# Performance work log

Measured on AMD Instinct MI355X. Metric: run time of the kernel, lower is better.

The kernel has to match this reference:

```python
import jax, jax.numpy as jnp
from jax import lax
import numpy as np

B, DIM, L_IN = 8, 512, 4096
SCALE = 2
KSIZE = 17
DN = ('NCH', 'OIH', 'NCH')  # conv1d dimension numbers


def _aa_kernel(kernel_size: int, scale: int) -> np.ndarray:
    # replicates scipy.signal.kaiser_atten / kaiser_beta / windows.kaiser
    atten = 2.285 * (kernel_size - 1) * np.pi * (1.0 / scale) + 7.95
    if atten > 50:
        beta = 0.1102 * (atten - 8.7)
    elif atten > 21:
        beta = 0.5842 * (atten - 21) ** 0.4 + 0.07886 * (atten - 21)
    else:
        beta = 0.0
    win = np.kaiser(kernel_size, beta)
    xk = np.arange(kernel_size) - kernel_size // 2
    k = np.sinc(xk / scale) * win  # normalized sinc, same as torch.sinc
    return (k / k.sum()).astype(np.float32)


def setup_inputs() -> dict:
    key = jax.random.key(0)
    k1, k2, k3, k4, k5 = jax.random.split(key, 5)
    kconv = 2 * SCALE - 1
    return {
        'x': jax.random.normal(k1, (B, DIM, L_IN), dtype=jnp.float32),
        'conv_w': jax.random.normal(k2, (DIM, DIM, kconv), dtype=jnp.float32) * (1.0 / np.sqrt(DIM * kconv)),
        'conv_b': jax.random.normal(k3, (DIM,), dtype=jnp.float32) * 0.01,
        'aa_kernel': jnp.asarray(_aa_kernel(KSIZE, SCALE)),
        'proj_w': jax.random.normal(k4, (DIM, DIM), dtype=jnp.float32) * (1.0 / np.sqrt(DIM)),
        'proj_b': jax.random.normal(k5, (DIM,), dtype=jnp.float32) * 0.01,
    }


def reference(x, conv_w, conv_b, aa_kernel, proj_w, proj_b):
    s = SCALE
    # zero-insertion upsample + Conv1d(dim,dim,2s-1,pad=s-1) fused via lhs_dilation.
    # Torch zero-inserts to length l*s (trailing s-1 zeros), so right pad is 2s-2.
    y = lax.conv_general_dilated(
        x, conv_w, window_strides=(1,), padding=[(s - 1, 2 * s - 2)],
        lhs_dilation=(s,), dimension_numbers=DN,
    ) + conv_b[None, :, None]  # [B, D, l*s]
    # depthwise anti-alias filter (same Kaiser-sinc kernel per channel)
    dw = jnp.broadcast_to(aa_kernel, (DIM, 1, KSIZE))
    y = lax.conv_general_dilated(
        y, dw, window_strides=(1,), padding=[(KSIZE // 2, KSIZE // 2)],
        feature_group_count=DIM, dimension_numbers=DN,
    )
    # pointwise 1x1 projection
    return jnp.einsum('bdl,ed->bel', y, proj_w) + proj_b[None, :, None]
```

## Files before the change

### kernel.cpp

```cpp
#include <hip/hip_runtime.h>
#include <hip/hip_bf16.h>

#define BB_   8
#define DIM_  512
#define LIN_  4096
#define LOUT_ 8192

typedef __attribute__((ext_vector_type(8))) __bf16 bf16x8;
typedef __attribute__((ext_vector_type(4))) float  f32x4;

__device__ __forceinline__ void async_copy16(const void* g, void* l) {
  __builtin_amdgcn_global_load_lds(
      (__attribute__((address_space(1))) void*)g,
      (__attribute__((address_space(3))) void*)l, 16, 0, 0);
}

__global__ __launch_bounds__(256) void k_transpose(const float* __restrict__ x,
                                                   __hip_bfloat16* __restrict__ Xt) {
  __shared__ float t[64][65];
  const int b  = blockIdx.x;
  const int d0 = blockIdx.y * 64;
  const int l0 = blockIdx.z * 64;
  const int tid = threadIdx.x;
  const int jj = tid & 63;
  const int i0 = tid >> 6;
#pragma unroll
  for (int r = 0; r < 16; ++r) {
    const int i = i0 + r * 4;
    t[i][jj] = x[(size_t)(b * DIM_ + d0 + i) * LIN_ + l0 + jj];
  }
  __syncthreads();
#pragma unroll
  for (int r = 0; r < 16; ++r) {
    const int i = i0 + r * 4;
    Xt[(size_t)(b * LIN_ + l0 + i) * DIM_ + d0 + jj] = __float2bfloat16(t[jj][i]);
  }
}

__global__ __launch_bounds__(256) void k_prep(const float* __restrict__ proj_w,
                                              const float* __restrict__ conv_w,
                                              __hip_bfloat16* __restrict__ Mst) {
  const int kk = blockIdx.x;
  const int et = blockIdx.y * 32;
  const int it = blockIdx.z * 32;
  __shared__ float Pt[32][33];
  __shared__ float Wt[32][33];
  const int tid = threadIdx.x;
  const int tx = tid & 15, ty = tid >> 4;
  float acc[2][2] = {};
  for (int d0 = 0; d0 < DIM_; d0 += 32) {
    {
      const int i = tid >> 3;
      const int j = (tid & 7) * 4;
      const float4 v = *(const float4*)&proj_w[(size_t)(et + i) * DIM_ + d0 + j];
      Pt[i][j] = v.x; Pt[i][j + 1] = v.y; Pt[i][j + 2] = v.z; Pt[i][j + 3] = v.w;
    }
#pragma unroll
    for (int r = 0; r < 4; ++r) {
      const int idx = tid + r * 256;
      const int i = idx >> 5, j = idx & 31;
      Wt[i][j] = conv_w[(size_t)(d0 + i) * (DIM_ * 3) + (it + j) * 3 + kk];
    }
    __syncthreads();
#pragma unroll
    for (int dl = 0; dl < 32; ++dl) {
      float pv[2], wv[2];
      pv[0] = Pt[ty * 2][dl];     pv[1] = Pt[ty * 2 + 1][dl];
      wv[0] = Wt[dl][tx * 2];     wv[1] = Wt[dl][tx * 2 + 1];
#pragma unroll
      for (int a = 0; a < 2; ++a)
#pragma unroll
        for (int bq = 0; bq < 2; ++bq) acc[a][bq] += pv[a] * wv[bq];
    }
    __syncthreads();
  }
#pragma unroll
  for (int a = 0; a < 2; ++a)
#pragma unroll
    for (int bq = 0; bq < 2; ++bq)
      Mst[(size_t)(kk * DIM_ + et + ty * 2 + a) * DIM_ + it + tx * 2 + bq] =
          __float2bfloat16(acc[a][bq]);
}

__global__ __launch_bounds__(64) void k_pcb(const float* __restrict__ proj_w,
                                            const float* __restrict__ conv_b,
                                            float* __restrict__ Pcb) {
  const int e = blockIdx.x;
  const int j = threadIdx.x;
  float s = 0.f;
#pragma unroll
  for (int d = j; d < DIM_; d += 64) s += proj_w[(size_t)e * DIM_ + d] * conv_b[d];
#pragma unroll
  for (int off = 32; off > 0; off >>= 1) s += __shfl_down(s, off, 64);
  if (j == 0) Pcb[e] = s;
}

__global__ __launch_bounds__(256) void k_gemm(const __hip_bfloat16* __restrict__ A,
                                              const __hip_bfloat16* __restrict__ Bt,
                                              const float* __restrict__ Pcb,
                                              __hip_bfloat16* __restrict__ U) {
  __shared__ __align__(16) __hip_bfloat16 As[128 * 64];
  __shared__ __align__(16) __hip_bfloat16 Bs[128 * 64];
  const int tid = threadIdx.x;
  const int r0 = blockIdx.x * 128;
  const int c0 = blockIdx.y * 128;
  const int lane = tid & 63;
  const int wave = tid >> 6;
  const int wm = wave >> 1, wn = wave & 1;

  const int srow = tid >> 3;
  const int cg   = (tid & 7) ^ (srow & 7);
  const __hip_bfloat16* aptr = A  + (size_t)(r0 + srow) * 512 + cg * 8;
  const __hip_bfloat16* bptr = Bt + (size_t)(c0 + srow) * 512 + cg * 8;
  __hip_bfloat16* ldsA = As + tid * 8;
  __hip_bfloat16* ldsB = Bs + tid * 8;

  f32x4 acc[4][4] = {};

  const int kq   = lane >> 4;
  const int mrow = wm * 64 + (lane & 15);
  const int ncol = wn * 64 + (lane & 15);

  for (int kt = 0; kt < 512; kt += 64) {
#pragma unroll
    for (int it = 0; it < 4; ++it) {
      async_copy16(aptr + (size_t)(it * 32) * 512 + kt, ldsA + it * 2048);
      async_copy16(bptr + (size_t)(it * 32) * 512 + kt, ldsB + it * 2048);
    }
    __syncthreads();
#pragma unroll
    for (int k0 = 0; k0 < 64; k0 += 32) {
      const int c = (k0 >> 3) + kq;
      bf16x8 af[4], bfr[4];
#pragma unroll
      for (int i = 0; i < 4; ++i) {
        const int rg = mrow + i * 16;
        af[i] = *(const bf16x8*)(As + rg * 64 + ((c ^ (rg & 7)) * 8));
      }
#pragma unroll
      for (int i = 0; i < 4; ++i) {
        const int rg = ncol + i * 16;
        bfr[i] = *(const bf16x8*)(Bs + rg * 64 + ((c ^ (rg & 7)) * 8));
      }
#pragma unroll
      for (int mt = 0; mt < 4; ++mt)
#pragma unroll
        for (int nt = 0; nt < 4; ++nt)
          acc[mt][nt] = __builtin_amdgcn_mfma_f32_16x16x32_bf16(af[mt], bfr[nt],
                                                                acc[mt][nt], 0, 0, 0);
    }
    __syncthreads();
  }

  const int kk = r0 >> 9;
  const int bb = c0 >> 12;
  const int e0 = (r0 & 511) + wm * 64;
  const int l0 = (c0 & 4095) + wn * 64;
#pragma unroll
  for (int mt = 0; mt < 4; ++mt) {
#pragma unroll
    for (int nt = 0; nt < 4; ++nt) {
      const int ltile = l0 + nt * 16 + (lane & 15);
      const int ebase = e0 + mt * 16 + (lane >> 4) * 4;
#pragma unroll
      for (int r = 0; r < 4; ++r) {
        float v = acc[mt][nt][r];
        const int e = ebase + r;
        if (kk < 2) v += Pcb[e];
        U[(size_t)((kk * 8 + bb) * 512 + e) * 4096 + ltile] = __float2bfloat16(v);
      }
    }
  }
}

__global__ __launch_bounds__(256) void k_aa(const __hip_bfloat16* __restrict__ U,
                                            const float* __restrict__ aa,
                                            const float* __restrict__ proj_b,
                                            float* __restrict__ out) {
  const int b  = blockIdx.x >> 9;
  const int e  = blockIdx.x & 511;
  const int l0 = blockIdx.y << 10;
  __shared__ __align__(16) float ue[1040];
  __shared__ __align__(16) float uo[1040];
  __shared__ float sa[17];
  const int tid = threadIdx.x;
  if (tid < 17) sa[tid] = aa[tid];
  const __hip_bfloat16* U0 = U + (size_t)((0 * 8 + b) * 512 + e) * 4096;
  const __hip_bfloat16* U1 = U + (size_t)((1 * 8 + b) * 512 + e) * 4096;
  const __hip_bfloat16* U2 = U + (size_t)((2 * 8 + b) * 512 + e) * 4096;
  for (int s = tid; s < 1040; s += 256) {
    const int l = l0 - 8 + s;
    float ve = 0.f, vo = 0.f;
    if (l >= 0 && l < 4096) {
      ve = __bfloat162float(U1[l]);
      vo = __bfloat162float(U0[l]);
      if (l + 1 < 4096) vo += __bfloat162float(U2[l + 1]);
    }
    ue[s] = ve;
    uo[s] = vo;
  }
  __syncthreads();
  const float pb = proj_b[e];
  const int li0 = tid * 4;
  const int w0  = li0 + 4;
  float Ew[12], Ow[12];
#pragma unroll
  for (int c = 0; c < 3; ++c) {
    const float4 ve = *(const float4*)&ue[w0 + 4 * c];
    const float4 vo = *(const float4*)&uo[w0 + 4 * c];
    Ew[4 * c] = ve.x; Ew[4 * c + 1] = ve.y; Ew[4 * c + 2] = ve.z; Ew[4 * c + 3] = ve.w;
    Ow[4 * c] = vo.x; Ow[4 * c + 1] = vo.y; Ow[4 * c + 2] = vo.z; Ow[4 * c + 3] = vo.w;
  }
  float res[8];
#pragma unroll
  for (int t = 0; t < 4; ++t) {
    float se = 0.f, so = 0.f;
#pragma unroll
    for (int q = 0; q <= 8; ++q) {
      se += sa[2 * q] * Ew[t + q];
      so += sa[2 * q] * Ow[t + q];
    }
#pragma unroll
    for (int q = 0; q < 8; ++q) {
      se += sa[2 * q + 1] * Ow[t + q];
      so += sa[2 * q + 1] * Ew[t + q + 1];
    }
    res[2 * t]     = se + pb;
    res[2 * t + 1] = so + pb;
  }
  float* orow = out + (size_t)(b * 512 + e) * 8192 + 2 * (l0 + li0);
  *(float4*)(orow)     = *(float4*)&res[0];
  *(float4*)(orow + 4) = *(float4*)&res[4];
}

extern "C" void kernel_launch(void* const* d_in, const int* in_sizes, int n_in,
                              void* d_out, int out_size, void* d_ws, size_t ws_size,
                              hipStream_t stream) {
  const float* x      = (const float*)d_in[0];
  const float* conv_w = (const float*)d_in[1];
  const float* conv_b = (const float*)d_in[2];
  const float* aa     = (const float*)d_in[3];
  const float* proj_w = (const float*)d_in[4];
  const float* proj_b = (const float*)d_in[5];
  float* out = (float*)d_out;

  char* ws = (char*)d_ws;
  __hip_bfloat16* Xt  = (__hip_bfloat16*)ws;
  __hip_bfloat16* Mst = (__hip_bfloat16*)(ws + 33554432);
  float*          Pcb = (float*)(ws + 35127296);
  __hip_bfloat16* U   = (__hip_bfloat16*)(ws + 35129344);

  k_transpose<<<dim3(8, 8, 64), 256, 0, stream>>>(x, Xt);
  k_prep<<<dim3(3, 16, 16), 256, 0, stream>>>(proj_w, conv_w, Mst);
  k_pcb<<<dim3(512, 1, 1), 64, 0, stream>>>(proj_w, conv_b, Pcb);
  k_gemm<<<dim3(12, 256), 256, 0, stream>>>(Mst, Xt, Pcb, U);
  k_aa<<<dim3(4096, 4), 256, 0, stream>>>(U, aa, proj_b, out);
}
```

Before: 384.5 us.

## Merge prep kernels, double-buffer GEMM LDS via registers, drop LDS staging in AA

Three preprocessing kernels (transpose, weight premultiply, bias projection) are merged into one launch that dispatches on block index, saving two launches. The GEMM swaps direct global-to-LDS async copies for register-staged loads into double-buffered LDS, so the next K tile is fetched while the current one is computed, at the cost of more LDS and a launch bound of two blocks. The anti-alias kernel now reads the bf16 intermediate straight into registers with vector loads and a fast-path bounds check instead of staging through shared memory. The block-index dispatch in the merged kernel must stay exact, and the extra LDS may limit occupancy.

New measurement: 380.7 us. No clear change (-1.0%).

```diff
diff --git a/kernel.cpp b/kernel.cpp
--- a/kernel.cpp
+++ b/kernel.cpp
@@ -9,98 +9,101 @@
 typedef __attribute__((ext_vector_type(8))) __bf16 bf16x8;
 typedef __attribute__((ext_vector_type(4))) float  f32x4;
 
-__device__ __forceinline__ void async_copy16(const void* g, void* l) {
-  __builtin_amdgcn_global_load_lds(
-      (__attribute__((address_space(1))) void*)g,
-      (__attribute__((address_space(3))) void*)l, 16, 0, 0);
-}
-
-__global__ __launch_bounds__(256) void k_transpose(const float* __restrict__ x,
-                                                   __hip_bfloat16* __restrict__ Xt) {
-  __shared__ float t[64][65];
-  const int b  = blockIdx.x;
-  const int d0 = blockIdx.y * 64;
-  const int l0 = blockIdx.z * 64;
+__device__ __forceinline__ float bf2f(unsigned short u) {
+  union { unsigned int i; float f; } x;
+  x.i = ((unsigned int)u) << 16;
+  return x.f;
+}
+
+__global__ __launch_bounds__(256) void k_pre(const float* __restrict__ x,
+                                             const float* __restrict__ proj_w,
+                                             const float* __restrict__ conv_w,
+                                             const float* __restrict__ conv_b,
+                                             __hip_bfloat16* __restrict__ Xt,
+                                             __hip_bfloat16* __restrict__ Mst,
+                                             float* __restrict__ Pcb) {
+  __shared__ float smem[64 * 65];
+  const int bx  = blockIdx.x;
   const int tid = threadIdx.x;
-  const int jj = tid & 63;
-  const int i0 = tid >> 6;
-#pragma unroll
-  for (int r = 0; r < 16; ++r) {
-    const int i = i0 + r * 4;
-    t[i][jj] = x[(size_t)(b * DIM_ + d0 + i) * LIN_ + l0 + jj];
-  }
-  __syncthreads();
-#pragma unroll
-  for (int r = 0; r < 16; ++r) {
-    const int i = i0 + r * 4;
-    Xt[(size_t)(b * LIN_ + l0 + i) * DIM_ + d0 + jj] = __float2bfloat16(t[jj][i]);
-  }
-}
-
-__global__ __launch_bounds__(256) void k_prep(const float* __restrict__ proj_w,
-                                              const float* __restrict__ conv_w,
-                                              __hip_bfloat16* __restrict__ Mst) {
-  const int kk = blockIdx.x;
-  const int et = blockIdx.y * 32;
-  const int it = blockIdx.z * 32;
-  __shared__ float Pt[32][33];
-  __shared__ float Wt[32][33];
-  const int tid = threadIdx.x;
-  const int tx = tid & 15, ty = tid >> 4;
-  float acc[2][2] = {};
-  for (int d0 = 0; d0 < DIM_; d0 += 32) {
-    {
-      const int i = tid >> 3;
-      const int j = (tid & 7) * 4;
-      const float4 v = *(const float4*)&proj_w[(size_t)(et + i) * DIM_ + d0 + j];
-      Pt[i][j] = v.x; Pt[i][j + 1] = v.y; Pt[i][j + 2] = v.z; Pt[i][j + 3] = v.w;
-    }
-#pragma unroll
-    for (int r = 0; r < 4; ++r) {
-      const int idx = tid + r * 256;
-      const int i = idx >> 5, j = idx & 31;
-      Wt[i][j] = conv_w[(size_t)(d0 + i) * (DIM_ * 3) + (it + j) * 3 + kk];
+  if (bx < 4096) {
+    const int b  = bx & 7;
+    const int d0 = ((bx >> 3) & 7) * 64;
+    const int l0 = (bx >> 6) * 64;
+    const int jj = tid & 63;
+    const int i0 = tid >> 6;
+#pragma unroll
+    for (int r = 0; r < 16; ++r) {
+      const int i = i0 + r * 4;
+      smem[i * 65 + jj] = x[(size_t)(b * DIM_ + d0 + i) * LIN_ + l0 + jj];
     }
     __syncthreads();
 #pragma unroll
-    for (int dl = 0; dl < 32; ++dl) {
-      float pv[2], wv[2];
-      pv[0] = Pt[ty * 2][dl];     pv[1] = Pt[ty * 2 + 1][dl];
-      wv[0] = Wt[dl][tx * 2];     wv[1] = Wt[dl][tx * 2 + 1];
-#pragma unroll
-      for (int a = 0; a < 2; ++a)
-#pragma unroll
-        for (int bq = 0; bq < 2; ++bq) acc[a][bq] += pv[a] * wv[bq];
-    }
-    __syncthreads();
-  }
-#pragma unroll
-  for (int a = 0; a < 2; ++a)
-#pragma unroll
-    for (int bq = 0; bq < 2; ++bq)
-      Mst[(size_t)(kk * DIM_ + et + ty * 2 + a) * DIM_ + it + tx * 2 + bq] =
-          __float2bfloat16(acc[a][bq]);
-}
-
-__global__ __launch_bounds__(64) void k_pcb(const float* __restrict__ proj_w,
-                                            const float* __restrict__ conv_b,
-                                            float* __restrict__ Pcb) {
-  const int e = blockIdx.x;
-  const int j = threadIdx.x;
-  float s = 0.f;
-#pragma unroll
-  for (int d = j; d < DIM_; d += 64) s += proj_w[(size_t)e * DIM_ + d] * conv_b[d];
-#pragma unroll
-  for (int off = 32; off > 0; off >>= 1) s += __shfl_down(s, off, 64);
-  if (j == 0) Pcb[e] = s;
-}
-
-__global__ __launch_bounds__(256) void k_gemm(const __hip_bfloat16* __restrict__ A,
-                                              const __hip_bfloat16* __restrict__ Bt,
-                                              const float* __restrict__ Pcb,
-                                              __hip_bfloat16* __restrict__ U) {
-  __shared__ __align__(16) __hip_bfloat16 As[128 * 64];
-  __shared__ __align__(16) __hip_bfloat16 Bs[128 * 64];
+    for (int r = 0; r < 16; ++r) {
+      const int i = i0 + r * 4;
+      Xt[(size_t)(b * LIN_ + l0 + i) * DIM_ + d0 + jj] =
+          __float2bfloat16(smem[jj * 65 + i]);
+    }
+  } else if (bx < 4864) {
+    const int idx = bx - 4096;
+    const int kk = idx >> 8;
+    const int et = ((idx >> 4) & 15) * 32;
+    const int it = (idx & 15) * 32;
+    float* Pt = smem;
+    float* Wt = smem + 32 * 33;
+    const int tx = tid & 15, ty = tid >> 4;
+    float acc[2][2] = {};
+    for (int d0 = 0; d0 < DIM_; d0 += 32) {
+      {
+        const int i = tid >> 3;
+        const int j = (tid & 7) * 4;
+        const float4 v = *(const float4*)&proj_w[(size_t)(et + i) * DIM_ + d0 + j];
+        Pt[i * 33 + j] = v.x; Pt[i * 33 + j + 1] = v.y;
+        Pt[i * 33 + j + 2] = v.z; Pt[i * 33 + j + 3] = v.w;
+      }
+#pragma unroll
+      for (int r = 0; r < 4; ++r) {
+        const int id2 = tid + r * 256;
+        const int i = id2 >> 5, j = id2 & 31;
+        Wt[i * 33 + j] = conv_w[(size_t)(d0 + i) * (DIM_ * 3) + (it + j) * 3 + kk];
+      }
+      __syncthreads();
+#pragma unroll
+      for (int dl = 0; dl < 32; ++dl) {
+        float pv[2], wv[2];
+        pv[0] = Pt[(ty * 2) * 33 + dl];     pv[1] = Pt[(ty * 2 + 1) * 33 + dl];
+        wv[0] = Wt[dl * 33 + tx * 2];       wv[1] = Wt[dl * 33 + tx * 2 + 1];
+#pragma unroll
+        for (int a = 0; a < 2; ++a)
+#pragma unroll
+          for (int bq = 0; bq < 2; ++bq) acc[a][bq] += pv[a] * wv[bq];
+      }
+      __syncthreads();
+    }
+#pragma unroll
+    for (int a = 0; a < 2; ++a)
+#pragma unroll
+      for (int bq = 0; bq < 2; ++bq)
+        Mst[(size_t)(kk * DIM_ + et + ty * 2 + a) * DIM_ + it + tx * 2 + bq] =
+            __float2bfloat16(acc[a][bq]);
+  } else {
+    const int idx = bx - 4864;
+    const int e = idx * 4 + (tid >> 6);
+    const int j = tid & 63;
+    float s = 0.f;
+#pragma unroll
+    for (int d = j; d < DIM_; d += 64) s += proj_w[(size_t)e * DIM_ + d] * conv_b[d];
+#pragma unroll
+    for (int off = 32; off > 0; off >>= 1) s += __shfl_down(s, off, 64);
+    if (j == 0) Pcb[e] = s;
+  }
+}
+
+__global__ __launch_bounds__(256, 2) void k_gemm(const __hip_bfloat16* __restrict__ A,
+                                                 const __hip_bfloat16* __restrict__ Bt,
+                                                 const float* __restrict__ Pcb,
+                                                 __hip_bfloat16* __restrict__ U) {
+  __shared__ __align__(16) __hip_bfloat16 As[2][128 * 64];
+  __shared__ __align__(16) __hip_bfloat16 Bs[2][128 * 64];
   const int tid = threadIdx.x;
   const int r0 = blockIdx.x * 128;
   const int c0 = blockIdx.y * 128;
@@ -108,26 +111,45 @@
   const int wave = tid >> 6;
   const int wm = wave >> 1, wn = wave & 1;
 
-  const int srow = tid >> 3;
-  const int cg   = (tid & 7) ^ (srow & 7);
-  const __hip_bfloat16* aptr = A  + (size_t)(r0 + srow) * 512 + cg * 8;
-  const __hip_bfloat16* bptr = Bt + (size_t)(c0 + srow) * 512 + cg * 8;
-  __hip_bfloat16* ldsA = As + tid * 8;
-  __hip_bfloat16* ldsB = Bs + tid * 8;
+  const int rA = tid >> 3;
+  const int ch = tid & 7;
+  const __hip_bfloat16* aG = A  + (size_t)(r0 + rA) * 512 + ch * 8;
+  const __hip_bfloat16* bG = Bt + (size_t)(c0 + rA) * 512 + ch * 8;
+  int wo[4];
+#pragma unroll
+  for (int i = 0; i < 4; ++i) {
+    const int rg = rA + 32 * i;
+    wo[i] = rg * 64 + ((ch ^ (rg & 7)) * 8);
+  }
+
+  bf16x8 gA[4], gB[4];
+#pragma unroll
+  for (int i = 0; i < 4; ++i) {
+    gA[i] = *(const bf16x8*)(aG + (size_t)(32 * i) * 512);
+    gB[i] = *(const bf16x8*)(bG + (size_t)(32 * i) * 512);
+  }
+#pragma unroll
+  for (int i = 0; i < 4; ++i) {
+    *(bf16x8*)(&As[0][wo[i]]) = gA[i];
+    *(bf16x8*)(&Bs[0][wo[i]]) = gB[i];
+  }
+  __syncthreads();
 
   f32x4 acc[4][4] = {};
-
   const int kq   = lane >> 4;
   const int mrow = wm * 64 + (lane & 15);
   const int ncol = wn * 64 + (lane & 15);
 
-  for (int kt = 0; kt < 512; kt += 64) {
-#pragma unroll
-    for (int it = 0; it < 4; ++it) {
-      async_copy16(aptr + (size_t)(it * 32) * 512 + kt, ldsA + it * 2048);
-      async_copy16(bptr + (size_t)(it * 32) * 512 + kt, ldsB + it * 2048);
-    }
-    __syncthreads();
+  for (int kt = 0; kt < 8; ++kt) {
+    if (kt < 7) {
+#pragma unroll
+      for (int i = 0; i < 4; ++i) {
+        gA[i] = *(const bf16x8*)(aG + (size_t)(32 * i) * 512 + (kt + 1) * 64);
+        gB[i] = *(const bf16x8*)(bG + (size_t)(32 * i) * 512 + (kt + 1) * 64);
+      }
+    }
+    const __hip_bfloat16* Ab = As[kt & 1];
+    const __hip_bfloat16* Bb = Bs[kt & 1];
 #pragma unroll
     for (int k0 = 0; k0 < 64; k0 += 32) {
       const int c = (k0 >> 3) + kq;
@@ -135,12 +157,12 @@
 #pragma unroll
       for (int i = 0; i < 4; ++i) {
         const int rg = mrow + i * 16;
-        af[i] = *(const bf16x8*)(As + rg * 64 + ((c ^ (rg & 7)) * 8));
+        af[i] = *(const bf16x8*)(Ab + rg * 64 + ((c ^ (rg & 7)) * 8));
       }
 #pragma unroll
       for (int i = 0; i < 4; ++i) {
         const int rg = ncol + i * 16;
-        bfr[i] = *(const bf16x8*)(Bs + rg * 64 + ((c ^ (rg & 7)) * 8));
+        bfr[i] = *(const bf16x8*)(Bb + rg * 64 + ((c ^ (rg & 7)) * 8));
       }
 #pragma unroll
       for (int mt = 0; mt < 4; ++mt)
@@ -148,6 +170,15 @@
         for (int nt = 0; nt < 4; ++nt)
           acc[mt][nt] = __builtin_amdgcn_mfma_f32_16x16x32_bf16(af[mt], bfr[nt],
                                                                 acc[mt][nt], 0, 0, 0);
+    }
+    if (kt < 7) {
+      __hip_bfloat16* wA = &As[(kt + 1) & 1][0];
+      __hip_bfloat16* wB = &Bs[(kt + 1) & 1][0];
+#pragma unroll
+      for (int i = 0; i < 4; ++i) {
+        *(bf16x8*)(&wA[wo[i]]) = gA[i];
+        *(bf16x8*)(&wB[wo[i]]) = gB[i];
+      }
     }
     __syncthreads();
   }
@@ -180,37 +211,51 @@
   const int b  = blockIdx.x >> 9;
   const int e  = blockIdx.x & 511;
   const int l0 = blockIdx.y << 10;
-  __shared__ __align__(16) float ue[1040];
-  __shared__ __align__(16) float uo[1040];
-  __shared__ float sa[17];
   const int tid = threadIdx.x;
-  if (tid < 17) sa[tid] = aa[tid];
-  const __hip_bfloat16* U0 = U + (size_t)((0 * 8 + b) * 512 + e) * 4096;
-  const __hip_bfloat16* U1 = U + (size_t)((1 * 8 + b) * 512 + e) * 4096;
-  const __hip_bfloat16* U2 = U + (size_t)((2 * 8 + b) * 512 + e) * 4096;
-  for (int s = tid; s < 1040; s += 256) {
-    const int l = l0 - 8 + s;
-    float ve = 0.f, vo = 0.f;
-    if (l >= 0 && l < 4096) {
-      ve = __bfloat162float(U1[l]);
-      vo = __bfloat162float(U0[l]);
-      if (l + 1 < 4096) vo += __bfloat162float(U2[l + 1]);
-    }
-    ue[s] = ve;
-    uo[s] = vo;
-  }
-  __syncthreads();
+  const int lt = l0 + 4 * tid;
+  const int w  = lt - 4;
+  const unsigned short* q0 = (const unsigned short*)(U + (size_t)((0 * 8 + b) * 512 + e) * 4096);
+  const unsigned short* q1 = (const unsigned short*)(U + (size_t)((1 * 8 + b) * 512 + e) * 4096);
+  const unsigned short* q2 = (const unsigned short*)(U + (size_t)((2 * 8 + b) * 512 + e) * 4096);
+
+  float Ew[12], Ow[12];
+  if (w >= 0 && w + 16 <= 4096) {
+    unsigned short e1[12], e0a[12], e2[16];
+#pragma unroll
+    for (int c = 0; c < 3; ++c) {
+      const ushort4 a = *(const ushort4*)(q1 + w + 4 * c);
+      e1[4 * c] = a.x; e1[4 * c + 1] = a.y; e1[4 * c + 2] = a.z; e1[4 * c + 3] = a.w;
+      const ushort4 d = *(const ushort4*)(q0 + w + 4 * c);
+      e0a[4 * c] = d.x; e0a[4 * c + 1] = d.y; e0a[4 * c + 2] = d.z; e0a[4 * c + 3] = d.w;
+    }
+#pragma unroll
+    for (int c = 0; c < 4; ++c) {
+      const ushort4 a = *(const ushort4*)(q2 + w + 4 * c);
+      e2[4 * c] = a.x; e2[4 * c + 1] = a.y; e2[4 * c + 2] = a.z; e2[4 * c + 3] = a.w;
+    }
+#pragma unroll
+    for (int j = 0; j < 12; ++j) {
+      Ew[j] = bf2f(e1[j]);
+      Ow[j] = bf2f(e0a[j]) + bf2f(e2[j + 1]);
+    }
+  } else {
+#pragma unroll
+    for (int j = 0; j < 12; ++j) {
+      const int l = w + j;
+      float vE = 0.f, vO = 0.f;
+      if (l >= 0 && l < 4096) {
+        vE = bf2f(q1[l]);
+        vO = bf2f(q0[l]);
+        if (l + 1 < 4096) vO += bf2f(q2[l + 1]);
+      }
+      Ew[j] = vE; Ow[j] = vO;
+    }
+  }
+
+  float sa[17];
+#pragma unroll
+  for (int j = 0; j < 17; ++j) sa[j] = aa[j];
   const float pb = proj_b[e];
-  const int li0 = tid * 4;
-  const int w0  = li0 + 4;
-  float Ew[12], Ow[12];
-#pragma unroll
-  for (int c = 0; c < 3; ++c) {
-    const float4 ve = *(const float4*)&ue[w0 + 4 * c];
-    const float4 vo = *(const float4*)&uo[w0 + 4 * c];
-    Ew[4 * c] = ve.x; Ew[4 * c + 1] = ve.y; Ew[4 * c + 2] = ve.z; Ew[4 * c + 3] = ve.w;
-    Ow[4 * c] = vo.x; Ow[4 * c + 1] = vo.y; Ow[4 * c + 2] = vo.z; Ow[4 * c + 3] = vo.w;
-  }
   float res[8];
 #pragma unroll
   for (int t = 0; t < 4; ++t) {
@@ -228,7 +273,7 @@
     res[2 * t]     = se + pb;
     res[2 * t + 1] = so + pb;
   }
-  float* orow = out + (size_t)(b * 512 + e) * 8192 + 2 * (l0 + li0);
+  float* orow = out + (size_t)(b * 512 + e) * 8192 + 2 * lt;
   *(float4*)(orow)     = *(float4*)&res[0];
   *(float4*)(orow + 4) = *(float4*)&res[4];
 }
@@ -250,9 +295,7 @@
   float*          Pcb = (float*)(ws + 35127296);
   __hip_bfloat16* U   = (__hip_bfloat16*)(ws + 35129344);
 
-  k_transpose<<<dim3(8, 8, 64), 256, 0, stream>>>(x, Xt);
-  k_prep<<<dim3(3, 16, 16), 256, 0, stream>>>(proj_w, conv_w, Mst);
-  k_pcb<<<dim3(512, 1, 1), 64, 0, stream>>>(proj_w, conv_b, Pcb);
+  k_pre<<<dim3(4992, 1, 1), 256, 0, stream>>>(x, proj_w, conv_w, conv_b, Xt, Mst, Pcb);
   k_gemm<<<dim3(12, 256), 256, 0, stream>>>(Mst, Xt, Pcb, U);
   k_aa<<<dim3(4096, 4), 256, 0, stream>>>(U, aa, proj_b, out);
 }
```
